# Performance work log

Hardware: AMD Instinct MI355X
Metric: run time of the kernel (lower is better)

Reference implementation:

```python
import jax, jax.numpy as jnp
import numpy as np

TOP_K = 2  # module default top_k


def setup_inputs() -> dict:
    key = jax.random.key(0)
    k1, k2, k3 = jax.random.split(key, 3)
    B, D, E = 4096, 1024, 64  # tokens, input_dim, num_experts
    return {
        "tensor1": jax.random.normal(k1, (B, D), dtype=jnp.float32),
        "tensor2": jax.random.normal(k2, (B, D), dtype=jnp.float32),
        "gate_weight": jax.random.normal(k3, (E, 2 * D), dtype=jnp.float32) * 0.02,
    }


def reference(tensor1, tensor2, gate_weight):
    # x: (B, 2D)
    x = jnp.concatenate((tensor1, tensor2), axis=-1)
    # pairwise L2 distance between each token and each expert vector
    diff = gate_weight[None, :, :] - x[:, None, :]          # (B, E, 2D)
    logits = -jnp.sqrt(jnp.sum(diff * diff, axis=-1))        # (B, E)
    topk_logits, indices = jax.lax.top_k(logits, TOP_K)      # (B, K)
    gating_weights = jax.nn.softmax(topk_logits, axis=-1)    # (B, K)
    rows = jnp.arange(logits.shape[0])[:, None]              # (B, 1)
    sparse_gating = jnp.zeros_like(logits).at[rows, indices].set(gating_weights)
    return sparse_gating
```

## Files before the change

kernel.cpp:

```cpp
#include <hip/hip_runtime.h>
#include <math.h>

#define NTOK 4096
#define NDIM 1024
#define KTOT 2048
#define NEXP 64
#define NWAVE 8
#define KCH  (KTOT / NWAVE)
#define NSTEP (KCH / 32)
#define RS   68

typedef _Float16 half8 __attribute__((ext_vector_type(8)));
typedef float    floatx4 __attribute__((ext_vector_type(4)));

#define XSCALE 16.0f
#define WSCALE 1024.0f
#define INVSCALE (1.0f / (16.0f * 1024.0f))

struct h2pair { _Float16 h, l; };
__device__ __forceinline__ h2pair split2(float v) {
    h2pair r;
    r.h = (_Float16)v;
    r.l = (_Float16)(v - (float)r.h);
    return r;
}

__global__ __launch_bounds__(256) void prep_w(const float* __restrict__ W,
                                              _Float16* __restrict__ WhT,
                                              _Float16* __restrict__ WlT,
                                              float* __restrict__ nrm) {
    const int e = blockIdx.x, t = threadIdx.x;
    const float* row = W + (size_t)e * KTOT + t * 8;
    const float4 a = *reinterpret_cast<const float4*>(row);
    const float4 b = *reinterpret_cast<const float4*>(row + 4);
    float ss = fmaf(a.x, a.x, fmaf(a.y, a.y, fmaf(a.z, a.z, fmaf(a.w, a.w, 0.f))));
    ss = fmaf(b.x, b.x, fmaf(b.y, b.y, fmaf(b.z, b.z, fmaf(b.w, b.w, ss))));

    const h2pair p0 = split2(a.x * WSCALE), p1 = split2(a.y * WSCALE);
    const h2pair p2 = split2(a.z * WSCALE), p3 = split2(a.w * WSCALE);
    const h2pair p4 = split2(b.x * WSCALE), p5 = split2(b.y * WSCALE);
    const h2pair p6 = split2(b.z * WSCALE), p7 = split2(b.w * WSCALE);
    half8 h, l;
    h[0]=p0.h; h[1]=p1.h; h[2]=p2.h; h[3]=p3.h; h[4]=p4.h; h[5]=p5.h; h[6]=p6.h; h[7]=p7.h;
    l[0]=p0.l; l[1]=p1.l; l[2]=p2.l; l[3]=p3.l; l[4]=p4.l; l[5]=p5.l; l[6]=p6.l; l[7]=p7.l;
    const size_t idx = ((size_t)t * NEXP + e) * 8;
    *reinterpret_cast<half8*>(WhT + idx) = h;
    *reinterpret_cast<half8*>(WlT + idx) = l;

    #pragma unroll
    for (int off = 32; off > 0; off >>= 1) ss += __shfl_down(ss, off, 64);
    __shared__ float red[4];
    const int lane = t & 63, wv = t >> 6;
    if (lane == 0) red[wv] = ss;
    __syncthreads();
    if (t == 0) nrm[e] = (red[0] + red[1]) + (red[2] + red[3]);
}

__global__ __launch_bounds__(512) void gate_fused(const float* __restrict__ t1,
                                                  const float* __restrict__ t2,
                                                  const _Float16* __restrict__ WhT,
                                                  const _Float16* __restrict__ WlT,
                                                  const float* __restrict__ nrm,
                                                  float* __restrict__ out) {
    __shared__ float Sd[NWAVE][16 * RS];
    __shared__ float Cn[NWAVE][16];

    const int tid  = threadIdx.x;
    const int lane = tid & 63;
    const int wv   = tid >> 6;
    const int tok0 = blockIdx.x * 16;
    const int kbase = wv * KCH;
    const int n  = lane & 15;
    const int fq = lane >> 4;

    const float* __restrict__ xb = ((kbase < NDIM)
        ? (t1 + (size_t)(tok0 + n) * NDIM + kbase)
        : (t2 + (size_t)(tok0 + n) * NDIM + (kbase - NDIM))) + fq * 8;
    const _Float16* __restrict__ whb = WhT + ((size_t)(kbase >> 3) + fq) * (NEXP * 8) + n * 8;
    const _Float16* __restrict__ wlb = WlT + ((size_t)(kbase >> 3) + fq) * (NEXP * 8) + n * 8;

    floatx4 acc[4];
    #pragma unroll
    for (int j = 0; j < 4; ++j) { acc[j][0]=0.f; acc[j][1]=0.f; acc[j][2]=0.f; acc[j][3]=0.f; }
    float ssx = 0.f;

    #pragma unroll
    for (int s = 0; s < NSTEP; ++s) {
        const float4 x0 = *reinterpret_cast<const float4*>(xb + s * 32);
        const float4 x1 = *reinterpret_cast<const float4*>(xb + s * 32 + 4);
        half8 bh[4], bl[4];
        #pragma unroll
        for (int j = 0; j < 4; ++j) {
            bh[j] = *reinterpret_cast<const half8*>(whb + (size_t)s * 4 * (NEXP * 8) + j * 128);
            bl[j] = *reinterpret_cast<const half8*>(wlb + (size_t)s * 4 * (NEXP * 8) + j * 128);
        }
        ssx = fmaf(x0.x, x0.x, fmaf(x0.y, x0.y, fmaf(x0.z, x0.z, fmaf(x0.w, x0.w, ssx))));
        ssx = fmaf(x1.x, x1.x, fmaf(x1.y, x1.y, fmaf(x1.z, x1.z, fmaf(x1.w, x1.w, ssx))));
        const h2pair q0 = split2(x0.x * XSCALE), q1 = split2(x0.y * XSCALE);
        const h2pair q2 = split2(x0.z * XSCALE), q3 = split2(x0.w * XSCALE);
        const h2pair q4 = split2(x1.x * XSCALE), q5 = split2(x1.y * XSCALE);
        const h2pair q6 = split2(x1.z * XSCALE), q7 = split2(x1.w * XSCALE);
        half8 ah, al;
        ah[0]=q0.h; ah[1]=q1.h; ah[2]=q2.h; ah[3]=q3.h; ah[4]=q4.h; ah[5]=q5.h; ah[6]=q6.h; ah[7]=q7.h;
        al[0]=q0.l; al[1]=q1.l; al[2]=q2.l; al[3]=q3.l; al[4]=q4.l; al[5]=q5.l; al[6]=q6.l; al[7]=q7.l;
        #pragma unroll
        for (int j = 0; j < 4; ++j)
            acc[j] = __builtin_amdgcn_mfma_f32_16x16x32_f16(ah, bh[j], acc[j], 0, 0, 0);
        #pragma unroll
        for (int j = 0; j < 4; ++j)
            acc[j] = __builtin_amdgcn_mfma_f32_16x16x32_f16(al, bh[j], acc[j], 0, 0, 0);
        #pragma unroll
        for (int j = 0; j < 4; ++j)
            acc[j] = __builtin_amdgcn_mfma_f32_16x16x32_f16(ah, bl[j], acc[j], 0, 0, 0);
    }

    #pragma unroll
    for (int j = 0; j < 4; ++j) {
        #pragma unroll
        for (int i = 0; i < 4; ++i)
            Sd[wv][(fq * 4 + i) * RS + 16 * j + n] = acc[j][i];
    }
    ssx += __shfl_xor(ssx, 16, 64);
    ssx += __shfl_xor(ssx, 32, 64);
    if (lane < 16) Cn[wv][lane] = ssx;
    __syncthreads();

    #pragma unroll
    for (int tt = 0; tt < 2; ++tt) {
        const int t = wv * 2 + tt;
        float gsum = 0.f, csum = 0.f;
        #pragma unroll
        for (int w = 0; w < NWAVE; ++w) {
            gsum += Sd[w][t * RS + lane];
            csum += Cn[w][t];
        }
        const float S = fmaf(-2.f * INVSCALE, gsum, csum) + nrm[lane];
        const float logit = -sqrtf(S);

        float v1 = logit; int i1 = lane;
        #pragma unroll
        for (int off = 32; off > 0; off >>= 1) {
            float ov = __shfl_xor(v1, off, 64);
            int   oi = __shfl_xor(i1, off, 64);
            if (ov > v1 || (ov == v1 && oi < i1)) { v1 = ov; i1 = oi; }
        }
        float v2 = (lane == i1) ? -__builtin_inff() : logit;
        int   i2 = lane;
        #pragma unroll
        for (int off = 32; off > 0; off >>= 1) {
            float ov = __shfl_xor(v2, off, 64);
            int   oi = __shfl_xor(i2, off, 64);
            if (ov > v2 || (ov == v2 && oi < i2)) { v2 = ov; i2 = oi; }
        }
        const float e2  = expf(v2 - v1);
        const float inv = 1.f / (1.f + e2);
        const float o = (lane == i1) ? inv : ((lane == i2) ? e2 * inv : 0.f);
        out[(size_t)(tok0 + t) * NEXP + lane] = o;
    }
}

extern "C" void kernel_launch(void* const* d_in, const int* in_sizes, int n_in,
                              void* d_out, int out_size, void* d_ws, size_t ws_size,
                              hipStream_t stream) {
    const float* t1 = (const float*)d_in[0];
    const float* t2 = (const float*)d_in[1];
    const float* W  = (const float*)d_in[2];
    float* out = (float*)d_out;

    char* ws = (char*)d_ws;
    float*    nrm = (float*)ws;
    _Float16* WhT = (_Float16*)(nrm + NEXP);
    _Float16* WlT = WhT + (size_t)NEXP * KTOT;

    prep_w<<<NEXP, 256, 0, stream>>>(W, WhT, WlT, nrm);
    gate_fused<<<NTOK / 16, 512, 0, stream>>>(t1, t2, WhT, WlT, nrm, out);
}
```

Measured before the change: 85.18 us.

## Split K across two blocks with 32-token tiles and add finalize kernel

Each block now processes 32 tokens over half of the K dimension, so every weight fragment loaded feeds two token sub-tiles. The K split keeps the block count the same. Partial dot products and input norms are written to workspace, and a new finalize kernel sums the two halves and does the sqrt, top-2 and softmax. This raises weight reuse per load at the cost of an extra kernel launch, extra global traffic for the partials, and more registers per wave.

```diff
diff --git a/kernel.cpp b/kernel.cpp
--- a/kernel.cpp
+++ b/kernel.cpp
@@ -5,10 +5,13 @@
 #define NDIM 1024
 #define KTOT 2048
 #define NEXP 64
+#define TPB_TOK 32
+#define KBLK 1024
 #define NWAVE 8
-#define KCH  (KTOT / NWAVE)
+#define KCH  (KBLK / NWAVE)
 #define NSTEP (KCH / 32)
 #define RS   68
+#define NTILE (NTOK / TPB_TOK)
 
 typedef _Float16 half8 __attribute__((ext_vector_type(8)));
 typedef float    floatx4 __attribute__((ext_vector_type(4)));
@@ -56,107 +59,153 @@
     if (t == 0) nrm[e] = (red[0] + red[1]) + (red[2] + red[3]);
 }
 
-__global__ __launch_bounds__(512) void gate_fused(const float* __restrict__ t1,
-                                                  const float* __restrict__ t2,
-                                                  const _Float16* __restrict__ WhT,
-                                                  const _Float16* __restrict__ WlT,
-                                                  const float* __restrict__ nrm,
-                                                  float* __restrict__ out) {
-    __shared__ float Sd[NWAVE][16 * RS];
-    __shared__ float Cn[NWAVE][16];
+__global__ __launch_bounds__(512) void gate_main(const float* __restrict__ t1,
+                                                 const float* __restrict__ t2,
+                                                 const _Float16* __restrict__ WhT,
+                                                 const _Float16* __restrict__ WlT,
+                                                 float* __restrict__ dotp,
+                                                 float* __restrict__ xnp) {
+    __shared__ float Sd[NWAVE][TPB_TOK * RS];
+    __shared__ float Cn[NWAVE][TPB_TOK];
 
     const int tid  = threadIdx.x;
     const int lane = tid & 63;
     const int wv   = tid >> 6;
-    const int tok0 = blockIdx.x * 16;
-    const int kbase = wv * KCH;
+    const int bid  = blockIdx.x;
+    const int tile = bid >> 1;
+    const int kb   = bid & 1;
+    const int tok0 = tile * TPB_TOK;
+    const int kbase = kb * KBLK + wv * KCH;
     const int n  = lane & 15;
     const int fq = lane >> 4;
 
-    const float* __restrict__ xb = ((kbase < NDIM)
-        ? (t1 + (size_t)(tok0 + n) * NDIM + kbase)
-        : (t2 + (size_t)(tok0 + n) * NDIM + (kbase - NDIM))) + fq * 8;
+    const float* __restrict__ xsrc = (kbase < NDIM) ? t1 : t2;
+    const int koff = (kbase < NDIM) ? kbase : (kbase - NDIM);
+    const float* __restrict__ xb0 = xsrc + (size_t)(tok0 + n) * NDIM + koff + fq * 8;
+    const float* __restrict__ xb1 = xsrc + (size_t)(tok0 + 16 + n) * NDIM + koff + fq * 8;
     const _Float16* __restrict__ whb = WhT + ((size_t)(kbase >> 3) + fq) * (NEXP * 8) + n * 8;
     const _Float16* __restrict__ wlb = WlT + ((size_t)(kbase >> 3) + fq) * (NEXP * 8) + n * 8;
 
-    floatx4 acc[4];
-    #pragma unroll
-    for (int j = 0; j < 4; ++j) { acc[j][0]=0.f; acc[j][1]=0.f; acc[j][2]=0.f; acc[j][3]=0.f; }
-    float ssx = 0.f;
+    floatx4 acc[2][4];
+    #pragma unroll
+    for (int tt = 0; tt < 2; ++tt)
+        #pragma unroll
+        for (int j = 0; j < 4; ++j) { acc[tt][j][0]=0.f; acc[tt][j][1]=0.f; acc[tt][j][2]=0.f; acc[tt][j][3]=0.f; }
+    float ss0a = 0.f, ss0b = 0.f, ss1a = 0.f, ss1b = 0.f;
 
     #pragma unroll
     for (int s = 0; s < NSTEP; ++s) {
-        const float4 x0 = *reinterpret_cast<const float4*>(xb + s * 32);
-        const float4 x1 = *reinterpret_cast<const float4*>(xb + s * 32 + 4);
+        const float4 x00 = *reinterpret_cast<const float4*>(xb0 + s * 32);
+        const float4 x01 = *reinterpret_cast<const float4*>(xb0 + s * 32 + 4);
+        const float4 x10 = *reinterpret_cast<const float4*>(xb1 + s * 32);
+        const float4 x11 = *reinterpret_cast<const float4*>(xb1 + s * 32 + 4);
         half8 bh[4], bl[4];
         #pragma unroll
         for (int j = 0; j < 4; ++j) {
             bh[j] = *reinterpret_cast<const half8*>(whb + (size_t)s * 4 * (NEXP * 8) + j * 128);
             bl[j] = *reinterpret_cast<const half8*>(wlb + (size_t)s * 4 * (NEXP * 8) + j * 128);
         }
-        ssx = fmaf(x0.x, x0.x, fmaf(x0.y, x0.y, fmaf(x0.z, x0.z, fmaf(x0.w, x0.w, ssx))));
-        ssx = fmaf(x1.x, x1.x, fmaf(x1.y, x1.y, fmaf(x1.z, x1.z, fmaf(x1.w, x1.w, ssx))));
-        const h2pair q0 = split2(x0.x * XSCALE), q1 = split2(x0.y * XSCALE);
-        const h2pair q2 = split2(x0.z * XSCALE), q3 = split2(x0.w * XSCALE);
-        const h2pair q4 = split2(x1.x * XSCALE), q5 = split2(x1.y * XSCALE);
-        const h2pair q6 = split2(x1.z * XSCALE), q7 = split2(x1.w * XSCALE);
-        half8 ah, al;
-        ah[0]=q0.h; ah[1]=q1.h; ah[2]=q2.h; ah[3]=q3.h; ah[4]=q4.h; ah[5]=q5.h; ah[6]=q6.h; ah[7]=q7.h;
-        al[0]=q0.l; al[1]=q1.l; al[2]=q2.l; al[3]=q3.l; al[4]=q4.l; al[5]=q5.l; al[6]=q6.l; al[7]=q7.l;
+        ss0a = fmaf(x00.x, x00.x, fmaf(x00.y, x00.y, fmaf(x00.z, x00.z, fmaf(x00.w, x00.w, ss0a))));
+        ss0b = fmaf(x01.x, x01.x, fmaf(x01.y, x01.y, fmaf(x01.z, x01.z, fmaf(x01.w, x01.w, ss0b))));
+        ss1a = fmaf(x10.x, x10.x, fmaf(x10.y, x10.y, fmaf(x10.z, x10.z, fmaf(x10.w, x10.w, ss1a))));
+        ss1b = fmaf(x11.x, x11.x, fmaf(x11.y, x11.y, fmaf(x11.z, x11.z, fmaf(x11.w, x11.w, ss1b))));
+        const h2pair q0 = split2(x00.x * XSCALE), q1 = split2(x00.y * XSCALE);
+        const h2pair q2 = split2(x00.z * XSCALE), q3 = split2(x00.w * XSCALE);
+        const h2pair q4 = split2(x01.x * XSCALE), q5 = split2(x01.y * XSCALE);
+        const h2pair q6 = split2(x01.z * XSCALE), q7 = split2(x01.w * XSCALE);
+        const h2pair r0 = split2(x10.x * XSCALE), r1 = split2(x10.y * XSCALE);
+        const h2pair r2 = split2(x10.z * XSCALE), r3 = split2(x10.w * XSCALE);
+        const h2pair r4 = split2(x11.x * XSCALE), r5 = split2(x11.y * XSCALE);
+        const h2pair r6 = split2(x11.z * XSCALE), r7 = split2(x11.w * XSCALE);
+        half8 ah0, al0, ah1, al1;
+        ah0[0]=q0.h; ah0[1]=q1.h; ah0[2]=q2.h; ah0[3]=q3.h; ah0[4]=q4.h; ah0[5]=q5.h; ah0[6]=q6.h; ah0[7]=q7.h;
+        al0[0]=q0.l; al0[1]=q1.l; al0[2]=q2.l; al0[3]=q3.l; al0[4]=q4.l; al0[5]=q5.l; al0[6]=q6.l; al0[7]=q7.l;
+        ah1[0]=r0.h; ah1[1]=r1.h; ah1[2]=r2.h; ah1[3]=r3.h; ah1[4]=r4.h; ah1[5]=r5.h; ah1[6]=r6.h; ah1[7]=r7.h;
+        al1[0]=r0.l; al1[1]=r1.l; al1[2]=r2.l; al1[3]=r3.l; al1[4]=r4.l; al1[5]=r5.l; al1[6]=r6.l; al1[7]=r7.l;
+        #pragma unroll
+        for (int j = 0; j < 4; ++j) {
+            acc[0][j] = __builtin_amdgcn_mfma_f32_16x16x32_f16(ah0, bh[j], acc[0][j], 0, 0, 0);
+            acc[1][j] = __builtin_amdgcn_mfma_f32_16x16x32_f16(ah1, bh[j], acc[1][j], 0, 0, 0);
+        }
+        #pragma unroll
+        for (int j = 0; j < 4; ++j) {
+            acc[0][j] = __builtin_amdgcn_mfma_f32_16x16x32_f16(al0, bh[j], acc[0][j], 0, 0, 0);
+            acc[1][j] = __builtin_amdgcn_mfma_f32_16x16x32_f16(al1, bh[j], acc[1][j], 0, 0, 0);
+        }
+        #pragma unroll
+        for (int j = 0; j < 4; ++j) {
+            acc[0][j] = __builtin_amdgcn_mfma_f32_16x16x32_f16(ah0, bl[j], acc[0][j], 0, 0, 0);
+            acc[1][j] = __builtin_amdgcn_mfma_f32_16x16x32_f16(ah1, bl[j], acc[1][j], 0, 0, 0);
+        }
+    }
+
+    #pragma unroll
+    for (int tt = 0; tt < 2; ++tt)
         #pragma unroll
         for (int j = 0; j < 4; ++j)
-            acc[j] = __builtin_amdgcn_mfma_f32_16x16x32_f16(ah, bh[j], acc[j], 0, 0, 0);
-        #pragma unroll
-        for (int j = 0; j < 4; ++j)
-            acc[j] = __builtin_amdgcn_mfma_f32_16x16x32_f16(al, bh[j], acc[j], 0, 0, 0);
-        #pragma unroll
-        for (int j = 0; j < 4; ++j)
-            acc[j] = __builtin_amdgcn_mfma_f32_16x16x32_f16(ah, bl[j], acc[j], 0, 0, 0);
-    }
-
-    #pragma unroll
-    for (int j = 0; j < 4; ++j) {
-        #pragma unroll
-        for (int i = 0; i < 4; ++i)
-            Sd[wv][(fq * 4 + i) * RS + 16 * j + n] = acc[j][i];
-    }
-    ssx += __shfl_xor(ssx, 16, 64);
-    ssx += __shfl_xor(ssx, 32, 64);
-    if (lane < 16) Cn[wv][lane] = ssx;
+            #pragma unroll
+            for (int i = 0; i < 4; ++i)
+                Sd[wv][(tt * 16 + fq * 4 + i) * RS + 16 * j + n] = acc[tt][j][i];
+
+    float ss0 = ss0a + ss0b, ss1 = ss1a + ss1b;
+    ss0 += __shfl_xor(ss0, 16, 64);
+    ss0 += __shfl_xor(ss0, 32, 64);
+    ss1 += __shfl_xor(ss1, 16, 64);
+    ss1 += __shfl_xor(ss1, 32, 64);
+    if (lane < 16) { Cn[wv][lane] = ss0; Cn[wv][16 + lane] = ss1; }
     __syncthreads();
 
     #pragma unroll
-    for (int tt = 0; tt < 2; ++tt) {
-        const int t = wv * 2 + tt;
+    for (int tt = 0; tt < 4; ++tt) {
+        const int t = wv * 4 + tt;
         float gsum = 0.f, csum = 0.f;
         #pragma unroll
         for (int w = 0; w < NWAVE; ++w) {
             gsum += Sd[w][t * RS + lane];
             csum += Cn[w][t];
         }
-        const float S = fmaf(-2.f * INVSCALE, gsum, csum) + nrm[lane];
-        const float logit = -sqrtf(S);
-
-        float v1 = logit; int i1 = lane;
-        #pragma unroll
-        for (int off = 32; off > 0; off >>= 1) {
-            float ov = __shfl_xor(v1, off, 64);
-            int   oi = __shfl_xor(i1, off, 64);
-            if (ov > v1 || (ov == v1 && oi < i1)) { v1 = ov; i1 = oi; }
-        }
-        float v2 = (lane == i1) ? -__builtin_inff() : logit;
-        int   i2 = lane;
-        #pragma unroll
-        for (int off = 32; off > 0; off >>= 1) {
-            float ov = __shfl_xor(v2, off, 64);
-            int   oi = __shfl_xor(i2, off, 64);
-            if (ov > v2 || (ov == v2 && oi < i2)) { v2 = ov; i2 = oi; }
-        }
-        const float e2  = expf(v2 - v1);
-        const float inv = 1.f / (1.f + e2);
-        const float o = (lane == i1) ? inv : ((lane == i2) ? e2 * inv : 0.f);
-        out[(size_t)(tok0 + t) * NEXP + lane] = o;
-    }
+        dotp[((size_t)(tile * 2 + kb) * TPB_TOK + t) * NEXP + lane] = gsum;
+        if (lane == 0) xnp[(size_t)(tile * 2 + kb) * TPB_TOK + t] = csum;
+    }
+}
+
+__global__ __launch_bounds__(512) void finalize(const float* __restrict__ dotp,
+                                                const float* __restrict__ xnp,
+                                                const float* __restrict__ nrm,
+                                                float* __restrict__ out) {
+    const int tid  = threadIdx.x;
+    const int lane = tid & 63;
+    const int wv   = tid >> 6;
+    const int tok  = blockIdx.x * 8 + wv;
+    const int tile = tok >> 5;
+    const int t    = tok & 31;
+
+    const float g = dotp[((size_t)(tile * 2 + 0) * TPB_TOK + t) * NEXP + lane]
+                  + dotp[((size_t)(tile * 2 + 1) * TPB_TOK + t) * NEXP + lane];
+    const float c = xnp[(size_t)(tile * 2 + 0) * TPB_TOK + t]
+                  + xnp[(size_t)(tile * 2 + 1) * TPB_TOK + t];
+    const float S = fmaf(-2.f * INVSCALE, g, c) + nrm[lane];
+    const float logit = -sqrtf(S);
+
+    float v1 = logit; int i1 = lane;
+    #pragma unroll
+    for (int off = 32; off > 0; off >>= 1) {
+        float ov = __shfl_xor(v1, off, 64);
+        int   oi = __shfl_xor(i1, off, 64);
+        if (ov > v1 || (ov == v1 && oi < i1)) { v1 = ov; i1 = oi; }
+    }
+    float v2 = (lane == i1) ? -__builtin_inff() : logit;
+    int   i2 = lane;
+    #pragma unroll
+    for (int off = 32; off > 0; off >>= 1) {
+        float ov = __shfl_xor(v2, off, 64);
+        int   oi = __shfl_xor(i2, off, 64);
+        if (ov > v2 || (ov == v2 && oi < i2)) { v2 = ov; i2 = oi; }
+    }
+    const float e2  = expf(v2 - v1);
+    const float inv = 1.f / (1.f + e2);
+    const float o = (lane == i1) ? inv : ((lane == i2) ? e2 * inv : 0.f);
+    out[(size_t)tok * NEXP + lane] = o;
 }
 
 extern "C" void kernel_launch(void* const* d_in, const int* in_sizes, int n_in,
@@ -168,10 +217,13 @@
     float* out = (float*)d_out;
 
     char* ws = (char*)d_ws;
-    float*    nrm = (float*)ws;
-    _Float16* WhT = (_Float16*)(nrm + NEXP);
-    _Float16* WlT = WhT + (size_t)NEXP * KTOT;
+    float*    nrm  = (float*)ws;
+    _Float16* WhT  = (_Float16*)(nrm + NEXP);
+    _Float16* WlT  = WhT + (size_t)NEXP * KTOT;
+    float*    dotp = (float*)(WlT + (size_t)NEXP * KTOT);
+    float*    xnp  = dotp + (size_t)NTILE * 2 * TPB_TOK * NEXP;
 
     prep_w<<<NEXP, 256, 0, stream>>>(W, WhT, WlT, nrm);
-    gate_fused<<<NTOK / 16, 512, 0, stream>>>(t1, t2, WhT, WlT, nrm, out);
-}
+    gate_main<<<NTILE * 2, 512, 0, stream>>>(t1, t2, WhT, WlT, dotp, xnp);
+    finalize<<<NTOK / 8, 512, 0, stream>>>(dotp, xnp, nrm, out);
+}
```

Measured after the change: 84.87 us, median of 2. No clear change (-0.4%).
